# Performance work log

Hardware: AMD Instinct MI355X
Metric: run time of the kernel (lower is better)

## Reference

```python
import jax, jax.numpy as jnp
import numpy as np

EPS = 1e-5

def binary_activation(x):
    # ReActNet piecewise-polynomial STE: forward = sign(x), grad follows poly
    m1 = (x < -1).astype(x.dtype)
    m2 = (x < 0).astype(x.dtype)
    m3 = (x < 1).astype(x.dtype)
    out1 = -1.0 * m1 + (x * x + 2.0 * x) * (1.0 - m1)
    out2 = out1 * m2 + (-x * x + 2.0 * x) * (1.0 - m2)
    out3 = out2 * m3 + 1.0 * (1.0 - m3)
    return jax.lax.stop_gradient(jnp.sign(x) - out3) + out3

def binary_conv(x, w, stride, padding):
    # per-output-channel scaled sign weights with clamp STE
    scale = jnp.mean(jnp.abs(w), axis=(1, 2, 3), keepdims=True)
    clipped = jnp.clip(w, -1.0, 1.0)
    bw = jax.lax.stop_gradient(scale * jnp.sign(w) - clipped) + clipped
    return jax.lax.conv_general_dilated(
        x, bw, window_strides=(stride, stride),
        padding=[(padding, padding), (padding, padding)],
        dimension_numbers=('NCHW', 'OIHW', 'NCHW'))

def batch_norm(x, g, b):
    mu = jnp.mean(x, axis=(0, 2, 3), keepdims=True)
    var = jnp.mean((x - mu) ** 2, axis=(0, 2, 3), keepdims=True)
    xn = (x - mu) * jax.lax.rsqrt(var + EPS)
    return xn * g[None, :, None, None] + b[None, :, None, None]

def prelu(x, a):
    a = a[None, :, None, None]
    return jnp.where(x >= 0, x, a * x)

def setup_inputs() -> dict:
    key = jax.random.key(0)
    ks = jax.random.split(key, 12)
    N, C, H, W = 32, 256, 56, 56
    d = {
        'x': jax.random.normal(ks[0], (N, C, H, W), jnp.float32),
        'b11': jax.random.normal(ks[1], (1, C, 1, 1), jnp.float32) * 0.1,
        'b12': jax.random.normal(ks[2], (1, C, 1, 1), jnp.float32) * 0.1,
        'b13': jax.random.normal(ks[3], (1, C, 1, 1), jnp.float32) * 0.1,
        'b21': jax.random.normal(ks[4], (1, C, 1, 1), jnp.float32) * 0.1,
        'b22': jax.random.normal(ks[5], (1, C, 1, 1), jnp.float32) * 0.1,
        'b23': jax.random.normal(ks[6], (1, C, 1, 1), jnp.float32) * 0.1,
        'w3x3': jax.random.normal(ks[7], (C, C, 3, 3), jnp.float32) * 0.05,
        'wpw': jax.random.normal(ks[8], (C, C, 1, 1), jnp.float32) * 0.05,
        'g1': jnp.ones((C,), jnp.float32),
        'be1': jnp.zeros((C,), jnp.float32),
        'g2': jnp.ones((C,), jnp.float32),
        'be2': jnp.zeros((C,), jnp.float32),
        'p1': jnp.full((C,), 0.25, jnp.float32),
        'p2': jnp.full((C,), 0.25, jnp.float32),
    }
    return d

def reference(x, b11, b12, b13, b21, b22, b23, w3x3, wpw, g1, be1, g2, be2, p1, p2):
    # stride=1, inplanes == planes branch
    out1 = binary_activation(x + b11)
    out1 = binary_conv(out1, w3x3, stride=1, padding=1)
    out1 = batch_norm(out1, g1, be1)
    out1 = x + out1
    out1 = prelu(out1 + b12, p1) + b13
    out2 = binary_activation(out1 + b21)
    out2 = binary_conv(out2, wpw, stride=1, padding=0)
    out2 = batch_norm(out2, g2, be2)
    out2 = out2 + out1
    out2 = prelu(out2 + b22, p2) + b23
    return out2
```

## Files before the change

### kernel.cpp

```cpp
#include <hip/hip_runtime.h>

typedef __attribute__((ext_vector_type(4))) float  f32x4;
typedef __attribute__((ext_vector_type(4))) short  s16x4;
typedef __attribute__((ext_vector_type(4))) int    i32x4;

#define MFMAI8(a, b, c) __builtin_amdgcn_mfma_i32_16x16x64_i8((a), (b), (c), 0, 0, 0)

__device__ __forceinline__ void gload_lds16(const void* g, void* l) {
  __builtin_amdgcn_global_load_lds((const __attribute__((address_space(1))) void*)g,
                                   (__attribute__((address_space(3))) void*)l, 16, 0, 0);
}

__device__ __forceinline__ char sgn8(float v) {
  return v > 0.f ? (char)1 : (v < 0.f ? (char)-1 : (char)0);
}

__global__ __launch_bounds__(256) void prep_w(const float* __restrict__ w3,
                                              const float* __restrict__ wpw,
                                              char* __restrict__ w1s,
                                              char* __restrict__ w2s,
                                              float* __restrict__ scale1,
                                              float* __restrict__ scale2) {
  const int o = blockIdx.x;
  const int t = threadIdx.x;
  float s = 0.f;
  if (blockIdx.y == 0) {
    for (int u = t; u < 2304; u += 256) {
      int i = u / 9, tap = u % 9;
      float v = w3[(size_t)(o * 256 + i) * 9 + tap];
      s += fabsf(v);
      w1s[(size_t)(tap * 256 + o) * 256 + i] = sgn8(v);
    }
  } else {
    float v = wpw[o * 256 + t];
    s = fabsf(v);
    w2s[o * 256 + t] = sgn8(v);
  }
  for (int m = 1; m < 64; m <<= 1) s += __shfl_xor(s, m);
  __shared__ float red[4];
  if ((t & 63) == 0) red[t >> 6] = s;
  __syncthreads();
  if (t == 0) {
    float tot = red[0] + red[1] + red[2] + red[3];
    if (blockIdx.y == 0) scale1[o] = tot / 2304.f;
    else                 scale2[o] = tot / 256.f;
  }
}

__global__ __launch_bounds__(256) void sign_nhwc(const float* __restrict__ x,
                                                 const float* __restrict__ b11,
                                                 char* __restrict__ out) {
  __shared__ unsigned short l[56 * 128];
  __shared__ float cB[256];
  const int h = blockIdx.x, n = blockIdx.y, t = threadIdx.x;
  cB[t] = b11[t];
  __syncthreads();
  const int wv = t & 15, cg = t >> 4;
  if (wv < 14) {
    const int w0 = wv * 4;
    const int swz = (wv & 7) << 3;
#pragma unroll 4
    for (int it = 0; it < 8; ++it) {
      int cp = it * 16 + cg;
      int c0 = cp * 2;
      size_t i0 = (size_t)(n * 256 + c0) * 3136 + h * 56 + w0;
      f32x4 x0 = *(const f32x4*)(x + i0);
      f32x4 x1 = *(const f32x4*)(x + i0 + 3136);
      float bb0 = cB[c0], bb1 = cB[c0 + 1];
      int cs = cp ^ swz;
#pragma unroll
      for (int j = 0; j < 4; ++j) {
        unsigned short pk = (unsigned char)sgn8(x0[j] + bb0) |
                            ((unsigned short)(unsigned char)sgn8(x1[j] + bb1) << 8);
        l[(w0 + j) * 128 + cs] = pk;
      }
    }
  }
  __syncthreads();
  char* op = out + ((size_t)(n * 56 + h) * 56) * 256;
  for (int u = t; u < 56 * 16; u += 256) {
    int w2 = u >> 4, cp = u & 15;
    *(i32x4*)(op + w2 * 256 + cp * 16) =
        *(const i32x4*)&l[w2 * 128 + ((cp * 8) ^ (((w2 >> 2) & 7) << 3))];
  }
}

__global__ __launch_bounds__(256, 2) void conv3x3(const char* __restrict__ sIn,
                                                  const char* __restrict__ wSgn,
                                                  short* __restrict__ raw,
                                                  long long* __restrict__ S,
                                                  long long* __restrict__ SS) {
  __shared__ char lin[4 * 58 * 256];

  int g = (blockIdx.x & 7) * 112 + (blockIdx.x >> 3);
  const int ht = g % 28, n = g / 28;
  const int h0 = ht * 2;

  const int t = threadIdx.x;
  const int lane = t & 63, wv = t >> 6;
  const int cl = lane & 15, kk = lane >> 4;

#pragma unroll
  for (int i = 0; i < 15; ++i) {
    int u = i * 256 + t;
    if (u < 3712) {
      int row = u / 928, rem = u % 928;
      int col = rem >> 4, sl = rem & 15;
      int h = h0 - 1 + row;
      int hc = min(max(h, 0), 55);
      int cc = min(max(col, 1), 56);
      const char* src = sIn + ((size_t)((n * 56 + hc) * 56 + (cc - 1)) << 8) +
                        ((sl ^ (col & 7)) << 4);
      gload_lds16(src, lin + u * 16);
    }
  }

  int r0[7], c0[7];
#pragma unroll
  for (int nf = 0; nf < 7; ++nf) {
    int p = nf * 16 + cl;
    r0[nf] = p / 56;
    c0[nf] = p % 56;
  }

  i32x4 acc[4][7];
#pragma unroll
  for (int m = 0; m < 4; ++m)
#pragma unroll
    for (int nf = 0; nf < 7; ++nf) acc[m][nf] = (i32x4){0, 0, 0, 0};

  const char* wbase = wSgn + (((size_t)(wv * 64 + cl)) << 8) + kk * 16;
#define WL(dst, kt_)                                                             \
  {                                                                              \
    const int icc_ = (kt_) / 9, tap_ = (kt_) % 9;                                \
    _Pragma("unroll")                                                            \
    for (int m_ = 0; m_ < 4; ++m_)                                               \
      dst[m_] = *(const i32x4*)(wbase + tap_ * 65536 + m_ * 4096 + icc_ * 64);   \
  }

  i32x4 wA[4], wB[4];
  WL(wA, 0);

  __syncthreads();

  if (t < 128) {
    int row = t >> 5, cs = (t >> 4) & 1, sl = t & 15;
    int col = cs ? 57 : 0;
    *(i32x4*)(lin + (row * 58 + col) * 256 + sl * 16) = (i32x4){0, 0, 0, 0};
  }
  if (h0 == 0) {
    for (int u = t; u < 928; u += 256)
      *(i32x4*)(lin + u * 16) = (i32x4){0, 0, 0, 0};
  }
  if (h0 == 54) {
    for (int u = t; u < 928; u += 256)
      *(i32x4*)(lin + (3 * 928 + u) * 16) = (i32x4){0, 0, 0, 0};
  }
  __syncthreads();

#pragma unroll
  for (int kt = 0; kt < 36; ++kt) {
    const int icc = kt / 9, tap = kt % 9;
    const int kh = tap / 3, kw = tap % 3;
    if (kt < 35) {
      if (kt & 1) { WL(wA, kt + 1); } else { WL(wB, kt + 1); }
    }
#pragma unroll
    for (int nf = 0; nf < 7; ++nf) {
      int col = c0[nf] + kw;
      int addr = ((r0[nf] + kh) * 58 + col) * 256 +
                 (((icc * 4 + kk) ^ (col & 7)) << 4);
      i32x4 b = *(const i32x4*)(lin + addr);
#pragma unroll
      for (int m = 0; m < 4; ++m) {
        if (kt & 1) acc[m][nf] = MFMAI8(wB[m], b, acc[m][nf]);
        else        acc[m][nf] = MFMAI8(wA[m], b, acc[m][nf]);
      }
    }
  }

  __syncthreads();
  unsigned short* tb = (unsigned short*)lin;
#pragma unroll
  for (int m = 0; m < 4; ++m) {
    int sm[4] = {0, 0, 0, 0};
    unsigned sq[4] = {0, 0, 0, 0};
#pragma unroll
    for (int nf = 0; nf < 7; ++nf) {
      i32x4 v = acc[m][nf];
#pragma unroll
      for (int r2 = 0; r2 < 4; ++r2) {
        sm[r2] += v[r2];
        sq[r2] += (unsigned)(v[r2] * v[r2]);
      }
    }
#pragma unroll
    for (int r2 = 0; r2 < 4; ++r2) {
      int aa = sm[r2];
      unsigned qq = sq[r2];
      aa += __shfl_xor(aa, 1); qq += __shfl_xor(qq, 1);
      aa += __shfl_xor(aa, 2); qq += __shfl_xor(qq, 2);
      aa += __shfl_xor(aa, 4); qq += __shfl_xor(qq, 4);
      aa += __shfl_xor(aa, 8); qq += __shfl_xor(qq, 8);
      if (cl == 0) {
        int oc = wv * 64 + m * 16 + kk * 4 + r2;
        atomicAdd((unsigned long long*)&S[oc], (unsigned long long)(long long)aa);
        atomicAdd((unsigned long long*)&SS[oc], (unsigned long long)qq);
      }
    }
    __syncthreads();
#pragma unroll
    for (int nf = 0; nf < 7; ++nf) {
      i32x4 v = acc[m][nf];
      int px = nf * 16 + cl;
#pragma unroll
      for (int r2 = 0; r2 < 4; ++r2)
        tb[(wv * 16 + kk * 4 + r2) * 120 + px] = (unsigned short)(short)v[r2];
    }
    __syncthreads();
#pragma unroll
    for (int i = 0; i < 4; ++i) {
      int u = i * 256 + t;
      int ocg = u >> 4, c8 = u & 15;
      if (c8 < 14) {
        int oc = (ocg >> 4) * 64 + m * 16 + (ocg & 15);
        *(i32x4*)(raw + ((size_t)n * 256 + oc) * 3136 + h0 * 56 + c8 * 8) =
            *(const i32x4*)&tb[ocg * 120 + c8 * 8];
      }
    }
  }
}

__global__ __launch_bounds__(256, 2) void conv1x1(const char* __restrict__ sIn,
                                                  const char* __restrict__ wSgn,
                                                  short* __restrict__ raw,
                                                  long long* __restrict__ S,
                                                  long long* __restrict__ SS) {
  __shared__ char lin[112 * 256];

  const int b = blockIdx.x;
  const int n = b / 28;
  const int hw0 = (b % 28) * 112;
  const size_t px0 = (size_t)n * 3136 + hw0;
  const int t = threadIdx.x, lane = t & 63, wv = t >> 6;
  const int cl = lane & 15, kk = lane >> 4;

#pragma unroll
  for (int i = 0; i < 7; ++i) {
    int u = i * 256 + t;
    int px = u >> 4, s = u & 15;
    const char* src = sIn + (px0 + px) * 256 + ((s ^ (px & 7)) * 16);
    gload_lds16(src, lin + u * 16);
  }

  i32x4 acc[4][7];
#pragma unroll
  for (int m = 0; m < 4; ++m)
#pragma unroll
    for (int nf = 0; nf < 7; ++nf) acc[m][nf] = (i32x4){0, 0, 0, 0};

  __syncthreads();

#pragma unroll
  for (int icc = 0; icc < 4; ++icc) {
    i32x4 bfr[7];
#pragma unroll
    for (int nf = 0; nf < 7; ++nf) {
      int px = nf * 16 + cl;
      int srd = (icc * 4 + kk) ^ (px & 7);
      bfr[nf] = *(const i32x4*)(lin + px * 256 + srd * 16);
    }
#pragma unroll
    for (int m = 0; m < 4; ++m) {
      i32x4 a = *(const i32x4*)(wSgn +
          (((size_t)(wv * 64 + m * 16 + cl)) << 8) + icc * 64 + kk * 16);
#pragma unroll
      for (int nf = 0; nf < 7; ++nf) acc[m][nf] = MFMAI8(a, bfr[nf], acc[m][nf]);
    }
  }

  __syncthreads();
  unsigned short* tb = (unsigned short*)lin;
#pragma unroll
  for (int m = 0; m < 4; ++m) {
    int sm[4] = {0, 0, 0, 0};
    unsigned sq[4] = {0, 0, 0, 0};
#pragma unroll
    for (int nf = 0; nf < 7; ++nf) {
      i32x4 v = acc[m][nf];
#pragma unroll
      for (int r2 = 0; r2 < 4; ++r2) {
        sm[r2] += v[r2];
        sq[r2] += (unsigned)(v[r2] * v[r2]);
      }
    }
#pragma unroll
    for (int r2 = 0; r2 < 4; ++r2) {
      int aa = sm[r2];
      unsigned qq = sq[r2];
      aa += __shfl_xor(aa, 1); qq += __shfl_xor(qq, 1);
      aa += __shfl_xor(aa, 2); qq += __shfl_xor(qq, 2);
      aa += __shfl_xor(aa, 4); qq += __shfl_xor(qq, 4);
      aa += __shfl_xor(aa, 8); qq += __shfl_xor(qq, 8);
      if (cl == 0) {
        int oc = wv * 64 + m * 16 + kk * 4 + r2;
        atomicAdd((unsigned long long*)&S[oc], (unsigned long long)(long long)aa);
        atomicAdd((unsigned long long*)&SS[oc], (unsigned long long)qq);
      }
    }
    __syncthreads();
#pragma unroll
    for (int nf = 0; nf < 7; ++nf) {
      i32x4 v = acc[m][nf];
      int px = nf * 16 + cl;
#pragma unroll
      for (int r2 = 0; r2 < 4; ++r2)
        tb[(wv * 16 + kk * 4 + r2) * 120 + px] = (unsigned short)(short)v[r2];
    }
    __syncthreads();
#pragma unroll
    for (int i = 0; i < 4; ++i) {
      int u = i * 256 + t;
      int ocg = u >> 4, c8 = u & 15;
      if (c8 < 14) {
        int oc = (ocg >> 4) * 64 + m * 16 + (ocg & 15);
        *(i32x4*)(raw + ((size_t)n * 256 + oc) * 3136 + hw0 + c8 * 8) =
            *(const i32x4*)&tb[ocg * 120 + c8 * 8];
      }
    }
  }
}

__global__ void bn_coef(const long long* __restrict__ S, const long long* __restrict__ SS,
                        const float* __restrict__ scale, const float* __restrict__ g,
                        const float* __restrict__ be, const float* __restrict__ bext,
                        float* __restrict__ A, float* __restrict__ B) {
  int o = threadIdx.x;
  const double invN = 1.0 / 100352.0;
  double mu_r  = (double)S[o] * invN;
  double var_r = (double)SS[o] * invN - mu_r * mu_r;
  double sc    = (double)scale[o];
  double rstd  = 1.0 / sqrt(sc * sc * var_r + 1e-5);
  double a     = (double)g[o] * rstd * sc;
  A[o] = (float)a;
  B[o] = (float)((double)be[o] - a * mu_r + (double)bext[o]);
}

__global__ __launch_bounds__(256) void mid_fuse(const short* __restrict__ raw,
                                                const float* __restrict__ x,
                                                const float* __restrict__ A1,
                                                const float* __restrict__ B1,
                                                const float* __restrict__ p1,
                                                const float* __restrict__ b13,
                                                const float* __restrict__ b21,
                                                float* __restrict__ t1,
                                                char* __restrict__ s2) {
  __shared__ unsigned short l[56 * 128];
  __shared__ float cA[256], cB[256], cP[256], cD[256], cE[256];
  const int h = blockIdx.x, n = blockIdx.y, t = threadIdx.x;
  cA[t] = A1[t]; cB[t] = B1[t]; cP[t] = p1[t]; cD[t] = b13[t]; cE[t] = b21[t];
  __syncthreads();
  const int wv = t & 15, cg = t >> 4;
  if (wv < 14) {
    const int w0 = wv * 4;
    const int swz = (wv & 7) << 3;
#pragma unroll 2
    for (int it = 0; it < 8; ++it) {
      int cp = it * 16 + cg;
      int c0 = cp * 2;
      size_t i0 = (size_t)(n * 256 + c0) * 3136 + h * 56 + w0;
      f32x4 x0 = *(const f32x4*)(x + i0);
      f32x4 x1 = *(const f32x4*)(x + i0 + 3136);
      s16x4 r0 = *(const s16x4*)(raw + i0);
      s16x4 r1 = *(const s16x4*)(raw + i0 + 3136);
      float a0 = cA[c0], b0 = cB[c0], p0 = cP[c0], d0 = cD[c0], e0 = cE[c0];
      float a1 = cA[c0+1], b1 = cB[c0+1], p1v = cP[c0+1], d1 = cD[c0+1], e1 = cE[c0+1];
      f32x4 o0, o1;
      int cs = cp ^ swz;
#pragma unroll
      for (int j = 0; j < 4; ++j) {
        float u0 = x0[j] + a0 * (float)r0[j] + b0;
        u0 = (u0 >= 0.f ? u0 : p0 * u0) + d0;
        o0[j] = u0;
        float u1 = x1[j] + a1 * (float)r1[j] + b1;
        u1 = (u1 >= 0.f ? u1 : p1v * u1) + d1;
        o1[j] = u1;
        unsigned short pk = (unsigned char)sgn8(u0 + e0) |
                            ((unsigned short)(unsigned char)sgn8(u1 + e1) << 8);
        l[(w0 + j) * 128 + cs] = pk;
      }
      *(f32x4*)(t1 + i0) = o0;
      *(f32x4*)(t1 + i0 + 3136) = o1;
    }
  }
  __syncthreads();
  char* op = s2 + ((size_t)(n * 56 + h) * 56) * 256;
  for (int u = t; u < 56 * 16; u += 256) {
    int w2 = u >> 4, cp = u & 15;
    *(i32x4*)(op + w2 * 256 + cp * 16) =
        *(const i32x4*)&l[w2 * 128 + ((cp * 8) ^ (((w2 >> 2) & 7) << 3))];
  }
}

__global__ __launch_bounds__(256) void final_fuse(const short* __restrict__ raw,
                                                  const float* __restrict__ A2,
                                                  const float* __restrict__ B2,
                                                  const float* __restrict__ p2,
                                                  const float* __restrict__ b23,
                                                  float* out) {
  const int c = blockIdx.x & 255;
  const size_t base = (size_t)blockIdx.x * 3136;
  const float a = A2[c], b = B2[c], p = p2[c], d = b23[c];
  for (int i = threadIdx.x; i < 784; i += 256) {
    s16x4 r  = *(const s16x4*)(raw + base + (size_t)i * 4);
    f32x4 tt = *(const f32x4*)(out + base + (size_t)i * 4);
    f32x4 o;
#pragma unroll
    for (int j = 0; j < 4; ++j) {
      float v = a * (float)r[j] + b + tt[j];
      o[j] = (v >= 0.f ? v : p * v) + d;
    }
    *(f32x4*)(out + base + (size_t)i * 4) = o;
  }
}

extern "C" void kernel_launch(void* const* d_in, const int* in_sizes, int n_in,
                              void* d_out, int out_size, void* d_ws, size_t ws_size,
                              hipStream_t stream) {
  const float* x   = (const float*)d_in[0];
  const float* b11 = (const float*)d_in[1];
  const float* b12 = (const float*)d_in[2];
  const float* b13 = (const float*)d_in[3];
  const float* b21 = (const float*)d_in[4];
  const float* b22 = (const float*)d_in[5];
  const float* b23 = (const float*)d_in[6];
  const float* w3  = (const float*)d_in[7];
  const float* wpw = (const float*)d_in[8];
  const float* g1  = (const float*)d_in[9];
  const float* be1 = (const float*)d_in[10];
  const float* g2  = (const float*)d_in[11];
  const float* be2 = (const float*)d_in[12];
  const float* p1  = (const float*)d_in[13];
  const float* p2  = (const float*)d_in[14];

  char* ws = (char*)d_ws;
  short*      raw    = (short*)(ws);
  char*       sgn    = (char*)(ws + 51380224);
  char*       w1s    = (char*)(ws + 77070336);
  char*       w2s    = (char*)(ws + 77660160);
  float*      scale1 = (float*)(ws + 77725696);
  float*      scale2 = (float*)(ws + 77726720);
  long long*  S1     = (long long*)(ws + 77727744);
  long long*  SS1    = (long long*)(ws + 77729792);
  long long*  S2     = (long long*)(ws + 77731840);
  long long*  SS2    = (long long*)(ws + 77733888);
  float*      A1     = (float*)(ws + 77735936);
  float*      B1     = (float*)(ws + 77736960);
  float*      A2     = (float*)(ws + 77737984);
  float*      B2     = (float*)(ws + 77739008);
  float*      t1     = (float*)d_out;

  hipMemsetAsync(ws + 77727744, 0, 8192, stream);

  prep_w<<<dim3(256, 2), 256, 0, stream>>>(w3, wpw, w1s, w2s, scale1, scale2);
  sign_nhwc<<<dim3(56, 32), 256, 0, stream>>>(x, b11, sgn);
  conv3x3<<<dim3(896), 256, 0, stream>>>(sgn, w1s, raw, S1, SS1);
  bn_coef<<<1, 256, 0, stream>>>(S1, SS1, scale1, g1, be1, b12, A1, B1);
  mid_fuse<<<dim3(56, 32), 256, 0, stream>>>(raw, x, A1, B1, p1, b13, b21, t1, sgn);
  conv1x1<<<dim3(896), 256, 0, stream>>>(sgn, w2s, raw, S2, SS2);
  bn_coef<<<1, 256, 0, stream>>>(S2, SS2, scale2, g2, be2, b22, A2, B2);
  final_fuse<<<dim3(8192), 256, 0, stream>>>(raw, A2, B2, p2, b23, (float*)d_out);
}
```

Before: 428.4 us.

## Pre-pack sign weights into MFMA fragment order and deepen weight prefetch

prep_w now writes the int8 sign weights in a fragment-major layout, so each lane's 16-byte A operand sits contiguously and a wave's load covers one 1 KB block. conv3x3 uses a three-buffer rotation that prefetches weights two k-steps ahead instead of one, to better hide global load latency behind the MFMAs. conv1x1 loads all its weight fragments into registers up front instead of loading them inside the reduction loop. The cost is more vector registers per thread, which could pressure occupancy under launch_bounds(256,2).

```diff
diff --git a/kernel.cpp b/kernel.cpp
--- a/kernel.cpp
+++ b/kernel.cpp
@@ -17,24 +17,27 @@
 
 __global__ __launch_bounds__(256) void prep_w(const float* __restrict__ w3,
                                               const float* __restrict__ wpw,
-                                              char* __restrict__ w1s,
-                                              char* __restrict__ w2s,
+                                              char* __restrict__ w1p,
+                                              char* __restrict__ w2p,
                                               float* __restrict__ scale1,
                                               float* __restrict__ scale2) {
   const int o = blockIdx.x;
   const int t = threadIdx.x;
+  const int oct = o >> 6, mo = (o >> 4) & 3, cl = o & 15;
   float s = 0.f;
   if (blockIdx.y == 0) {
     for (int u = t; u < 2304; u += 256) {
       int i = u / 9, tap = u % 9;
       float v = w3[(size_t)(o * 256 + i) * 9 + tap];
       s += fabsf(v);
-      w1s[(size_t)(tap * 256 + o) * 256 + i] = sgn8(v);
+      size_t frag = (size_t)(tap * 4 + (i >> 6)) * 16 + oct * 4 + mo;
+      w1p[frag * 1024 + ((i >> 4) & 3) * 256 + cl * 16 + (i & 15)] = sgn8(v);
     }
   } else {
     float v = wpw[o * 256 + t];
     s = fabsf(v);
-    w2s[o * 256 + t] = sgn8(v);
+    size_t frag = (size_t)((t >> 6) * 4 + oct) * 4 + mo;
+    w2p[frag * 1024 + ((t >> 4) & 3) * 256 + cl * 16 + (t & 15)] = sgn8(v);
   }
   for (int m = 1; m < 64; m <<= 1) s += __shfl_xor(s, m);
   __shared__ float red[4];
@@ -86,7 +89,7 @@
 }
 
 __global__ __launch_bounds__(256, 2) void conv3x3(const char* __restrict__ sIn,
-                                                  const char* __restrict__ wSgn,
+                                                  const char* __restrict__ w1p,
                                                   short* __restrict__ raw,
                                                   long long* __restrict__ S,
                                                   long long* __restrict__ SS) {
@@ -129,17 +132,18 @@
 #pragma unroll
     for (int nf = 0; nf < 7; ++nf) acc[m][nf] = (i32x4){0, 0, 0, 0};
 
-  const char* wbase = wSgn + (((size_t)(wv * 64 + cl)) << 8) + kk * 16;
+  const char* wpb = w1p + (size_t)wv * 4 * 1024 + lane * 16;
 #define WL(dst, kt_)                                                             \
   {                                                                              \
     const int icc_ = (kt_) / 9, tap_ = (kt_) % 9;                                \
     _Pragma("unroll")                                                            \
     for (int m_ = 0; m_ < 4; ++m_)                                               \
-      dst[m_] = *(const i32x4*)(wbase + tap_ * 65536 + m_ * 4096 + icc_ * 64);   \
-  }
-
-  i32x4 wA[4], wB[4];
+      dst[m_] = *(const i32x4*)(wpb + ((size_t)(tap_ * 4 + icc_) * 16 + m_) * 1024); \
+  }
+
+  i32x4 wA[4], wB[4], wC[4];
   WL(wA, 0);
+  WL(wB, 1);
 
   __syncthreads();
 
@@ -158,25 +162,31 @@
   }
   __syncthreads();
 
+#define CMP(wsel)                                                                \
+  {                                                                              \
+    _Pragma("unroll")                                                            \
+    for (int nf = 0; nf < 7; ++nf) {                                             \
+      int col = c0[nf] + kw;                                                     \
+      int addr = ((r0[nf] + kh) * 58 + col) * 256 +                              \
+                 (((icc * 4 + kk) ^ (col & 7)) << 4);                            \
+      i32x4 b = *(const i32x4*)(lin + addr);                                     \
+      _Pragma("unroll")                                                          \
+      for (int m = 0; m < 4; ++m) acc[m][nf] = MFMAI8(wsel[m], b, acc[m][nf]);   \
+    }                                                                            \
+  }
+
 #pragma unroll
   for (int kt = 0; kt < 36; ++kt) {
     const int icc = kt / 9, tap = kt % 9;
     const int kh = tap / 3, kw = tap % 3;
-    if (kt < 35) {
-      if (kt & 1) { WL(wA, kt + 1); } else { WL(wB, kt + 1); }
-    }
-#pragma unroll
-    for (int nf = 0; nf < 7; ++nf) {
-      int col = c0[nf] + kw;
-      int addr = ((r0[nf] + kh) * 58 + col) * 256 +
-                 (((icc * 4 + kk) ^ (col & 7)) << 4);
-      i32x4 b = *(const i32x4*)(lin + addr);
-#pragma unroll
-      for (int m = 0; m < 4; ++m) {
-        if (kt & 1) acc[m][nf] = MFMAI8(wB[m], b, acc[m][nf]);
-        else        acc[m][nf] = MFMAI8(wA[m], b, acc[m][nf]);
-      }
-    }
+    if (kt < 34) {
+      if (kt % 3 == 0)      { WL(wC, kt + 2); }
+      else if (kt % 3 == 1) { WL(wA, kt + 2); }
+      else                  { WL(wB, kt + 2); }
+    }
+    if (kt % 3 == 0)      { CMP(wA) }
+    else if (kt % 3 == 1) { CMP(wB) }
+    else                  { CMP(wC) }
   }
 
   __syncthreads();
@@ -232,7 +242,7 @@
 }
 
 __global__ __launch_bounds__(256, 2) void conv1x1(const char* __restrict__ sIn,
-                                                  const char* __restrict__ wSgn,
+                                                  const char* __restrict__ w2p,
                                                   short* __restrict__ raw,
                                                   long long* __restrict__ S,
                                                   long long* __restrict__ SS) {
@@ -253,6 +263,14 @@
     gload_lds16(src, lin + u * 16);
   }
 
+  i32x4 wreg[4][4];
+#pragma unroll
+  for (int icc = 0; icc < 4; ++icc)
+#pragma unroll
+    for (int m = 0; m < 4; ++m)
+      wreg[icc][m] = *(const i32x4*)(w2p +
+          ((size_t)((icc * 4 + wv) * 4 + m)) * 1024 + lane * 16);
+
   i32x4 acc[4][7];
 #pragma unroll
   for (int m = 0; m < 4; ++m)
@@ -271,12 +289,10 @@
       bfr[nf] = *(const i32x4*)(lin + px * 256 + srd * 16);
     }
 #pragma unroll
-    for (int m = 0; m < 4; ++m) {
-      i32x4 a = *(const i32x4*)(wSgn +
-          (((size_t)(wv * 64 + m * 16 + cl)) << 8) + icc * 64 + kk * 16);
-#pragma unroll
-      for (int nf = 0; nf < 7; ++nf) acc[m][nf] = MFMAI8(a, bfr[nf], acc[m][nf]);
-    }
+    for (int m = 0; m < 4; ++m)
+#pragma unroll
+      for (int nf = 0; nf < 7; ++nf)
+        acc[m][nf] = MFMAI8(wreg[icc][m], bfr[nf], acc[m][nf]);
   }
 
   __syncthreads();
@@ -446,8 +462,8 @@
   char* ws = (char*)d_ws;
   short*      raw    = (short*)(ws);
   char*       sgn    = (char*)(ws + 51380224);
-  char*       w1s    = (char*)(ws + 77070336);
-  char*       w2s    = (char*)(ws + 77660160);
+  char*       w1p    = (char*)(ws + 77070336);
+  char*       w2p    = (char*)(ws + 77660160);
   float*      scale1 = (float*)(ws + 77725696);
   float*      scale2 = (float*)(ws + 77726720);
   long long*  S1     = (long long*)(ws + 77727744);
@@ -462,12 +478,12 @@
 
   hipMemsetAsync(ws + 77727744, 0, 8192, stream);
 
-  prep_w<<<dim3(256, 2), 256, 0, stream>>>(w3, wpw, w1s, w2s, scale1, scale2);
+  prep_w<<<dim3(256, 2), 256, 0, stream>>>(w3, wpw, w1p, w2p, scale1, scale2);
   sign_nhwc<<<dim3(56, 32), 256, 0, stream>>>(x, b11, sgn);
-  conv3x3<<<dim3(896), 256, 0, stream>>>(sgn, w1s, raw, S1, SS1);
+  conv3x3<<<dim3(896), 256, 0, stream>>>(sgn, w1p, raw, S1, SS1);
   bn_coef<<<1, 256, 0, stream>>>(S1, SS1, scale1, g1, be1, b12, A1, B1);
   mid_fuse<<<dim3(56, 32), 256, 0, stream>>>(raw, x, A1, B1, p1, b13, b21, t1, sgn);
-  conv1x1<<<dim3(896), 256, 0, stream>>>(sgn, w2s, raw, S2, SS2);
+  conv1x1<<<dim3(896), 256, 0, stream>>>(sgn, w2p, raw, S2, SS2);
   bn_coef<<<1, 256, 0, stream>>>(S2, SS2, scale2, g2, be2, b22, A2, B2);
   final_fuse<<<dim3(8192), 256, 0, stream>>>(raw, A2, B2, p2, b23, (float*)d_out);
 }
```

Measured after the change: 405.4 us. 5.3% less time.
